# Kernel tuning notes

Measured on AMD Instinct MI355X. Metric: run time of the kernel, lower is better.

## Reference

```python
import jax, jax.numpy as jnp
import numpy as np

N = 200000   # nodes
E = 6400000  # edges (avg degree 32)
T = 6        # member feature dim
M = 10       # fingerprint dim
L = 4        # R + 1 layers
GIN = 14     # group_level_input
GLO = 10     # group_level_output


def setup_inputs() -> dict:
    key = jax.random.key(0)
    ks = jax.random.split(key, 10)
    return {
        "x_member": jax.random.normal(ks[0], (N, T), dtype=jnp.float32),
        "x_group": jax.random.normal(ks[1], (1, GIN), dtype=jnp.float32),
        "src": jax.random.randint(ks[2], (E,), 0, N, dtype=jnp.int32),
        "dst": jax.random.randint(ks[3], (E,), 0, N, dtype=jnp.int32),
        "H": jax.random.normal(ks[4], (L, T, M), dtype=jnp.float32),
        "W": jax.random.normal(ks[5], (L,), dtype=jnp.float32),
        "gW": jax.random.normal(ks[6], (GLO, GIN), dtype=jnp.float32) * 0.1,
        "gb": jax.random.normal(ks[7], (GLO,), dtype=jnp.float32),
        "mW": jax.random.normal(ks[8], (3, M + GLO), dtype=jnp.float32) * 0.1,
        "mb": jax.random.normal(ks[9], (3,), dtype=jnp.float32),
    }


def reference(x_member, x_group, src, dst, H, W, gW, gb, mW, mb):
    n = x_member.shape[0]
    # message passing: neighbor feature sum per destination node  [N, T]
    neigh = jax.ops.segment_sum(x_member[src], dst, num_segments=n)
    v1 = x_member + neigh  # r[a] + sum of neighbor r's; r is layer-invariant
    # all R+1 layers at once: [L, N, M]
    v2 = jax.nn.sigmoid(jnp.einsum("nt,ltm->lnm", v1, H))
    fl = jax.nn.softmax(v2 * W[:, None, None], axis=-1)
    # f starts at zeros and accumulates softmax over every node and layer -> [1, M]
    f = jnp.sum(fl, axis=(0, 1))[None, :]
    # group-level perceptron
    g = jax.nn.sigmoid(x_group @ gW.T + gb)  # [1, GLO]
    merged = jnp.concatenate([f, g], axis=1)  # [1, M+GLO]
    return jax.nn.softmax(merged @ mW.T + mb, axis=-1)  # [1, 3]
```

## Files before the change

kernel.cpp:

```cpp
#include <hip/hip_runtime.h>
#include <hip/hip_fp16.h>
#include <math.h>

#define TDIM 6
#define MDIM 10
#define LDIM 4
#define GIND 14
#define GLOD 10

#define BINSHIFT 8
#define BINSZ 256
#define MAXBINS 1024

#define SC2_BLOCKS 512
#define SC2_THREADS 512
#define SC2_KQ 7
#define OVF_ENT 16384
#define META2 2048

#define SC_BLOCK 512
#define SC_EPT 32
#define SC_EPB (SC_BLOCK * SC_EPT)
#define AC_BLOCK 512
#define AC_CAP 8704
#define AC_EPT 17

typedef unsigned uvec4_t __attribute__((ext_vector_type(4)));

__device__ __forceinline__ void add_row4(uint4 r, float& s0, float& s1, float& s2,
                                         float& s3, float& s4, float& s5) {
    float2 a0 = __half22float2(*(__half2*)&r.x);
    float2 a1 = __half22float2(*(__half2*)&r.y);
    float2 a2 = __half22float2(*(__half2*)&r.z);
    s0 += a0.x; s1 += a0.y; s2 += a1.x; s3 += a1.y; s4 += a2.x; s5 += a2.y;
}

__global__ void zero32_k(unsigned* __restrict__ p, int n) {
    int i = blockIdx.x * blockDim.x + threadIdx.x;
    if (i < n) p[i] = 0u;
}


__global__ __launch_bounds__(SC2_THREADS) void scat2_k(
        const float* __restrict__ xm, int N, uint4* __restrict__ xh,
        const int* __restrict__ src, const int* __restrict__ dst, int E, int NQ, int QPB,
        unsigned* __restrict__ gcount, unsigned* __restrict__ ebuf, int C, int nbins,
        uint2* __restrict__ ovf, unsigned* __restrict__ ocur) {
    __shared__ unsigned lcount[MAXBINS];
    __shared__ unsigned lbase[MAXBINS];
    int tid = threadIdx.x;
    for (int i = tid; i < MAXBINS; i += SC2_THREADS) lcount[i] = 0u;

    int gid = blockIdx.x * SC2_THREADS + tid;
    int gstride = gridDim.x * SC2_THREADS;
    for (int n = gid; n < N; n += gstride) {
        const float2* r = (const float2*)(xm + (size_t)n * TDIM);
        float2 a = r[0], b = r[1], c = r[2];
        __half2 h0 = __floats2half2_rn(a.x, a.y);
        __half2 h1 = __floats2half2_rn(b.x, b.y);
        __half2 h2 = __floats2half2_rn(c.x, c.y);
        uint4 o;
        o.x = *(unsigned*)&h0; o.y = *(unsigned*)&h1; o.z = *(unsigned*)&h2; o.w = 0u;
        xh[n] = o;
    }
    if (blockIdx.x == 0) {
        for (int e = NQ * 4 + tid; e < E; e += SC2_THREADS) {
            unsigned oc = atomicAdd(ocur, 1u);
            if (oc < OVF_ENT) ovf[oc] = make_uint2((unsigned)src[e], (unsigned)dst[e]);
        }
    }
    __syncthreads();

    int qb = blockIdx.x * QPB;
    int qend = qb + QPB; if (qend > NQ) qend = NQ;
    const int4* s4p = (const int4*)src;
    const int4* d4p = (const int4*)dst;

    unsigned pk[SC2_KQ * 4];
    unsigned wr[SC2_KQ * 4];

#pragma unroll
    for (int i = 0; i < SC2_KQ; i++) {
        int q = qb + tid + i * SC2_THREADS;
        if (q < qend) {
            int4 sv = s4p[q];
            int4 dv = d4p[q];
            {
                unsigned du = (unsigned)dv.x, b = du >> BINSHIFT;
                pk[i*4+0] = ((du & (BINSZ-1)) << 18) | (unsigned)sv.x;
                wr[i*4+0] = (b << 18) | atomicAdd(&lcount[b], 1u);
            }
            {
                unsigned du = (unsigned)dv.y, b = du >> BINSHIFT;
                pk[i*4+1] = ((du & (BINSZ-1)) << 18) | (unsigned)sv.y;
                wr[i*4+1] = (b << 18) | atomicAdd(&lcount[b], 1u);
            }
            {
                unsigned du = (unsigned)dv.z, b = du >> BINSHIFT;
                pk[i*4+2] = ((du & (BINSZ-1)) << 18) | (unsigned)sv.z;
                wr[i*4+2] = (b << 18) | atomicAdd(&lcount[b], 1u);
            }
            {
                unsigned du = (unsigned)dv.w, b = du >> BINSHIFT;
                pk[i*4+3] = ((du & (BINSZ-1)) << 18) | (unsigned)sv.w;
                wr[i*4+3] = (b << 18) | atomicAdd(&lcount[b], 1u);
            }
        } else {
            pk[i*4+0] = 0xFFFFFFFFu; pk[i*4+1] = 0xFFFFFFFFu;
            pk[i*4+2] = 0xFFFFFFFFu; pk[i*4+3] = 0xFFFFFFFFu;
        }
    }
    __syncthreads();

    for (int i = tid; i < nbins; i += SC2_THREADS) {
        unsigned c = lcount[i];
        if (c) lbase[i] = atomicAdd(&gcount[i], c);
    }
    __syncthreads();

#pragma unroll
    for (int k = 0; k < SC2_KQ * 4; k++) {
        unsigned p = pk[k];
        if (p != 0xFFFFFFFFu) {
            unsigned b = wr[k] >> 18;
            unsigned pos = lbase[b] + (wr[k] & 0x3FFFFu);
            if (pos < (unsigned)C) {
                ebuf[b * (unsigned)C + pos] = p;
            } else {
                unsigned oc = atomicAdd(ocur, 1u);
                if (oc < OVF_ENT) {
                    unsigned s = p & 0x3FFFFu;
                    unsigned d = (b << BINSHIFT) | (p >> 18);
                    ovf[oc] = make_uint2(s, d);
                }
            }
        }
    }
}

__global__ __launch_bounds__(AC_BLOCK) void accum2_k(
        const float* __restrict__ xm, const uint4* __restrict__ xh,
        const unsigned* __restrict__ ebuf, const unsigned* __restrict__ gcount, int C,
        const unsigned* __restrict__ ocur, const uint2* __restrict__ ovf,
        const float* __restrict__ H, const float* __restrict__ W,
        float* __restrict__ facc, int N) {
    __shared__ unsigned srt[AC_CAP];
    __shared__ unsigned cnt[BINSZ];
    __shared__ unsigned tmp[BINSZ];
    __shared__ unsigned cstart[BINSZ];
    __shared__ unsigned ovl[256];
    __shared__ unsigned ovn;
    __shared__ float sH[LDIM * TDIM * MDIM];
    __shared__ float sW[LDIM];
    __shared__ float sred[AC_BLOCK / 64][MDIM];
    __shared__ float part[2][BINSZ][TDIM];
    int tid = threadIdx.x;
    int bin = blockIdx.x;
    for (int i = tid; i < LDIM * TDIM * MDIM; i += AC_BLOCK) sH[i] = H[i];
    if (tid < LDIM) sW[tid] = W[tid];
    if (tid < BINSZ) cnt[tid] = 0u;
    if (tid == 0) ovn = 0u;
    __syncthreads();

    unsigned gc = gcount[bin];
    unsigned m = gc < (unsigned)C ? gc : (unsigned)C;
    unsigned e0 = (unsigned)bin * (unsigned)C;
    int nbase = bin << BINSHIFT;

    unsigned ed_[AC_EPT];
    unsigned rk_[AC_EPT];
#pragma unroll
    for (int k = 0; k < AC_EPT; k++) {
        unsigned i = (unsigned)tid + (unsigned)k * AC_BLOCK;
        if (i < m) {
            unsigned v = __builtin_nontemporal_load(ebuf + e0 + i);
            ed_[k] = v;
            rk_[k] = atomicAdd(&cnt[v >> 18], 1u);
        }
    }
    {
        unsigned novf = *ocur;
        if (novf > OVF_ENT) novf = OVF_ENT;
        for (unsigned i = tid; i < novf; i += AC_BLOCK) {
            uint2 e = ovf[i];
            if ((e.y >> BINSHIFT) == (unsigned)bin) {
                unsigned u = atomicAdd(&ovn, 1u);
                if (u < 256u) ovl[u] = ((e.y & (BINSZ-1)) << 18) | e.x;
            }
        }
    }
    __syncthreads();

    if (tid < BINSZ) tmp[tid] = cnt[tid];
    __syncthreads();
    for (int off = 1; off < BINSZ; off <<= 1) {
        unsigned v = 0;
        if (tid < BINSZ) { v = tmp[tid]; if (tid >= off) v += tmp[tid - off]; }
        __syncthreads();
        if (tid < BINSZ) tmp[tid] = v;
        __syncthreads();
    }
    if (tid < BINSZ) cstart[tid] = tmp[tid] - cnt[tid];
    __syncthreads();

#pragma unroll
    for (int k = 0; k < AC_EPT; k++) {
        unsigned i = (unsigned)tid + (unsigned)k * AC_BLOCK;
        if (i < m) {
            unsigned v = ed_[k];
            srt[cstart[v >> 18] + rk_[k]] = v & 0x3FFFFu;
        }
    }
    __syncthreads();

    int node = tid & (BINSZ - 1);
    int role = tid >> 8;
    int n = nbase + node;
    float s0 = 0.f, s1 = 0.f, s2 = 0.f, s3 = 0.f, s4 = 0.f, s5 = 0.f;
    if (n < N) {
        unsigned c = cnt[node];
        unsigned b0 = cstart[node];
        unsigned h = c >> 1;
        unsigned j  = role ? h : 0u;
        unsigned je = role ? c : h;
        for (; j + 4 <= je; j += 4) {
            unsigned ia = srt[b0 + j],     ib = srt[b0 + j + 1];
            unsigned ic = srt[b0 + j + 2], id = srt[b0 + j + 3];
            uint4 ra = xh[ia];
            uint4 rb = xh[ib];
            uint4 rc = xh[ic];
            uint4 rd = xh[id];
            add_row4(ra, s0, s1, s2, s3, s4, s5);
            add_row4(rb, s0, s1, s2, s3, s4, s5);
            add_row4(rc, s0, s1, s2, s3, s4, s5);
            add_row4(rd, s0, s1, s2, s3, s4, s5);
        }
        for (; j < je; ++j) {
            uint4 ra = xh[srt[b0 + j]];
            add_row4(ra, s0, s1, s2, s3, s4, s5);
        }
        if (role == 0) {
            unsigned no = ovn < 256u ? ovn : 256u;
            for (unsigned q = 0; q < no; q++) {
                unsigned o = ovl[q];
                if ((int)(o >> 18) == node) {
                    uint4 rr = xh[o & 0x3FFFFu];
                    add_row4(rr, s0, s1, s2, s3, s4, s5);
                }
            }
        }
    }
    part[role][node][0] = s0; part[role][node][1] = s1; part[role][node][2] = s2;
    part[role][node][3] = s3; part[role][node][4] = s4; part[role][node][5] = s5;
    __syncthreads();

    float fs[MDIM];
#pragma unroll
    for (int mm = 0; mm < MDIM; mm++) fs[mm] = 0.f;

    if (n < N) {
        float v[TDIM];
        const float2* xr = (const float2*)(xm + (size_t)n * TDIM);
        float2 x0 = xr[0], x1 = xr[1], x2 = xr[2];
        v[0] = x0.x + part[0][node][0] + part[1][node][0];
        v[1] = x0.y + part[0][node][1] + part[1][node][1];
        v[2] = x1.x + part[0][node][2] + part[1][node][2];
        v[3] = x1.y + part[0][node][3] + part[1][node][3];
        v[4] = x2.x + part[0][node][4] + part[1][node][4];
        v[5] = x2.y + part[0][node][5] + part[1][node][5];

        int lb = role << 1;
#pragma unroll
        for (int li = 0; li < 2; li++) {
            int l = lb + li;
            float z[MDIM];
#pragma unroll
            for (int mm = 0; mm < MDIM; mm++) {
                float a2 = 0.f;
#pragma unroll
                for (int t = 0; t < TDIM; t++) a2 += v[t] * sH[(l * TDIM + t) * MDIM + mm];
                z[mm] = a2;
            }
            float wl = sW[l];
            float mx = -1e30f;
#pragma unroll
            for (int mm = 0; mm < MDIM; mm++) {
                float sg = wl / (1.f + __expf(-z[mm]));
                z[mm] = sg;
                mx = fmaxf(mx, sg);
            }
            float se = 0.f;
#pragma unroll
            for (int mm = 0; mm < MDIM; mm++) {
                float e = __expf(z[mm] - mx);
                z[mm] = e;
                se += e;
            }
            float inv = 1.f / se;
#pragma unroll
            for (int mm = 0; mm < MDIM; mm++) fs[mm] += z[mm] * inv;
        }
    }

#pragma unroll
    for (int mm = 0; mm < MDIM; mm++) {
        float v = fs[mm];
#pragma unroll
        for (int off = 32; off > 0; off >>= 1) v += __shfl_down(v, off, 64);
        fs[mm] = v;
    }
    int wave = tid >> 6, lane = tid & 63;
    if (lane == 0) {
#pragma unroll
        for (int mm = 0; mm < MDIM; mm++) sred[wave][mm] = fs[mm];
    }
    __syncthreads();
    if (tid < MDIM) {
        float s = 0.f;
#pragma unroll
        for (int w = 0; w < AC_BLOCK / 64; w++) s += sred[w][tid];
        atomicAdd(facc + tid, s);
    }
}


__global__ __launch_bounds__(256) void prep_k(const float* __restrict__ xm, int N,
                                              uint4* __restrict__ xh,
                                              const int* __restrict__ dst, int E,
                                              unsigned* __restrict__ hist, int nbins) {
    __shared__ unsigned lh[MAXBINS];
    for (int i = threadIdx.x; i < MAXBINS; i += blockDim.x) lh[i] = 0u;
    __syncthreads();
    int gid = blockIdx.x * blockDim.x + threadIdx.x;
    int gstride = gridDim.x * blockDim.x;
    for (int n = gid; n < N; n += gstride) {
        const float2* r = (const float2*)(xm + (size_t)n * TDIM);
        float2 a = r[0], b = r[1], c = r[2];
        __half2 h0 = __floats2half2_rn(a.x, a.y);
        __half2 h1 = __floats2half2_rn(b.x, b.y);
        __half2 h2 = __floats2half2_rn(c.x, c.y);
        uint4 o;
        o.x = *(unsigned*)&h0; o.y = *(unsigned*)&h1; o.z = *(unsigned*)&h2; o.w = 0u;
        xh[n] = o;
    }
    int e4 = E >> 2;
    const int4* d4p = (const int4*)dst;
    for (int i = gid; i < e4; i += gstride) {
        int4 d = d4p[i];
        atomicAdd(&lh[((unsigned)d.x) >> BINSHIFT], 1u);
        atomicAdd(&lh[((unsigned)d.y) >> BINSHIFT], 1u);
        atomicAdd(&lh[((unsigned)d.z) >> BINSHIFT], 1u);
        atomicAdd(&lh[((unsigned)d.w) >> BINSHIFT], 1u);
    }
    for (int e = (e4 << 2) + gid; e < E; e += gstride)
        atomicAdd(&lh[((unsigned)dst[e]) >> BINSHIFT], 1u);
    __syncthreads();
    for (int i = threadIdx.x; i < nbins; i += blockDim.x)
        if (lh[i]) atomicAdd(&hist[i], lh[i]);
}

__global__ __launch_bounds__(MAXBINS) void scan_k(const unsigned* __restrict__ hist,
                                                  unsigned* __restrict__ offsets,
                                                  unsigned* __restrict__ gfill, int nbins) {
    __shared__ unsigned buf[2][MAXBINS];
    int t = threadIdx.x;
    buf[0][t] = (t < nbins) ? hist[t] : 0u;
    __syncthreads();
    int cur = 0;
    for (int off = 1; off < MAXBINS; off <<= 1) {
        unsigned v = buf[cur][t];
        if (t >= off) v += buf[cur][t - off];
        buf[cur ^ 1][t] = v;
        __syncthreads();
        cur ^= 1;
    }
    if (t < nbins) {
        unsigned ex = t ? buf[cur][t - 1] : 0u;
        offsets[t] = ex;
        gfill[t] = ex;
    }
    if (t == 0) offsets[nbins] = buf[cur][nbins - 1];
}

__global__ __launch_bounds__(SC_BLOCK) void scatter_k(const int* __restrict__ src,
                                                      const int* __restrict__ dst, int E,
                                                      unsigned* __restrict__ gfill,
                                                      unsigned* __restrict__ ebuf, int nbins) {
    __shared__ unsigned lcount[MAXBINS];
    __shared__ unsigned lbase[MAXBINS];
    for (int i = threadIdx.x; i < MAXBINS; i += SC_BLOCK) lcount[i] = 0u;
    __syncthreads();
    int base = blockIdx.x * SC_EPB + threadIdx.x * SC_EPT;
    int s[SC_EPT], d[SC_EPT];
    unsigned rk[SC_EPT];
#pragma unroll
    for (int q = 0; q < SC_EPT / 4; q++) {
        int e = base + q * 4;
        if (e + 3 < E) {
            int4 s4 = *(const int4*)(src + e);
            int4 d4 = *(const int4*)(dst + e);
            s[q*4+0] = s4.x; s[q*4+1] = s4.y; s[q*4+2] = s4.z; s[q*4+3] = s4.w;
            d[q*4+0] = d4.x; d[q*4+1] = d4.y; d[q*4+2] = d4.z; d[q*4+3] = d4.w;
        } else {
#pragma unroll
            for (int k = 0; k < 4; k++) {
                int ee = e + k;
                s[q*4+k] = (ee < E) ? src[ee] : -1;
                d[q*4+k] = (ee < E) ? dst[ee] : 0;
            }
        }
    }
#pragma unroll
    for (int k = 0; k < SC_EPT; k++)
        if (s[k] >= 0) rk[k] = atomicAdd(&lcount[((unsigned)d[k]) >> BINSHIFT], 1u);
    __syncthreads();
    for (int i = threadIdx.x; i < nbins; i += SC_BLOCK) {
        unsigned c = lcount[i];
        if (c) lbase[i] = atomicAdd(&gfill[i], c);
    }
    __syncthreads();
#pragma unroll
    for (int k = 0; k < SC_EPT; k++) {
        if (s[k] >= 0) {
            unsigned du = (unsigned)d[k];
            unsigned b = du >> BINSHIFT;
            unsigned pack = ((du & (BINSZ - 1)) << 18) | (unsigned)s[k];
            ebuf[lbase[b] + rk[k]] = pack;
        }
    }
}

__global__ __launch_bounds__(AC_BLOCK) void accum_node_k(
        const float* __restrict__ xm, const uint4* __restrict__ xh,
        const unsigned* __restrict__ ebuf, const unsigned* __restrict__ offsets,
        const float* __restrict__ H, const float* __restrict__ W,
        float* __restrict__ facc, int N) {
    __shared__ unsigned srt[AC_CAP];
    __shared__ unsigned cnt[BINSZ];
    __shared__ unsigned tmp[BINSZ];
    __shared__ unsigned cstart[BINSZ];
    __shared__ float sH[LDIM * TDIM * MDIM];
    __shared__ float sW[LDIM];
    __shared__ float sred[AC_BLOCK / 64][MDIM];
    int tid = threadIdx.x;
    int bin = blockIdx.x;
    for (int i = tid; i < LDIM * TDIM * MDIM; i += AC_BLOCK) sH[i] = H[i];
    if (tid < LDIM) sW[tid] = W[tid];
    if (tid < BINSZ) cnt[tid] = 0u;
    __syncthreads();

    unsigned e0 = offsets[bin], e1 = offsets[bin + 1];
    unsigned total = e1 - e0;
    unsigned m = total < AC_CAP ? total : AC_CAP;
    int nbase = bin << BINSHIFT;

    unsigned ed_[AC_EPT];
    unsigned rk_[AC_EPT];
#pragma unroll
    for (int k = 0; k < AC_EPT; k++) {
        unsigned idx = e0 + (unsigned)tid + (unsigned)k * AC_BLOCK;
        if (idx < e0 + m) {
            unsigned v = ebuf[idx];
            ed_[k] = v;
            rk_[k] = atomicAdd(&cnt[v >> 18], 1u);
        }
    }
    __syncthreads();

    if (tid < BINSZ) tmp[tid] = cnt[tid];
    __syncthreads();
    for (int off = 1; off < BINSZ; off <<= 1) {
        unsigned v = 0;
        if (tid < BINSZ) { v = tmp[tid]; if (tid >= off) v += tmp[tid - off]; }
        __syncthreads();
        if (tid < BINSZ) tmp[tid] = v;
        __syncthreads();
    }
    if (tid < BINSZ) cstart[tid] = tmp[tid] - cnt[tid];
    __syncthreads();

#pragma unroll
    for (int k = 0; k < AC_EPT; k++) {
        unsigned idx = e0 + (unsigned)tid + (unsigned)k * AC_BLOCK;
        if (idx < e0 + m) {
            unsigned v = ed_[k];
            srt[cstart[v >> 18] + rk_[k]] = v & 0x3FFFFu;
        }
    }
    __syncthreads();

    float fs[MDIM];
#pragma unroll
    for (int mm = 0; mm < MDIM; mm++) fs[mm] = 0.f;

    int n = nbase + tid;
    if (tid < BINSZ && n < N) {
        float s0 = 0.f, s1 = 0.f, s2 = 0.f, s3 = 0.f, s4 = 0.f, s5 = 0.f;
        unsigned c = cnt[tid];
        unsigned b0 = cstart[tid];
        unsigned j = 0;
        for (; j + 2 <= c; j += 2) {
            unsigned sa = srt[b0 + j], sb = srt[b0 + j + 1];
            uint4 ra = xh[sa];
            uint4 rb = xh[sb];
            float2 a0 = __half22float2(*(__half2*)&ra.x);
            float2 a1 = __half22float2(*(__half2*)&ra.y);
            float2 a2 = __half22float2(*(__half2*)&ra.z);
            float2 c0 = __half22float2(*(__half2*)&rb.x);
            float2 c1 = __half22float2(*(__half2*)&rb.y);
            float2 c2 = __half22float2(*(__half2*)&rb.z);
            s0 += a0.x + c0.x; s1 += a0.y + c0.y;
            s2 += a1.x + c1.x; s3 += a1.y + c1.y;
            s4 += a2.x + c2.x; s5 += a2.y + c2.y;
        }
        if (j < c) {
            uint4 ra = xh[srt[b0 + j]];
            float2 a0 = __half22float2(*(__half2*)&ra.x);
            float2 a1 = __half22float2(*(__half2*)&ra.y);
            float2 a2 = __half22float2(*(__half2*)&ra.z);
            s0 += a0.x; s1 += a0.y; s2 += a1.x; s3 += a1.y; s4 += a2.x; s5 += a2.y;
        }
        for (unsigned idx = e0 + m; idx < e1; idx++) {
            unsigned v = ebuf[idx];
            if ((int)(v >> 18) == tid) {
                uint4 ra = xh[v & 0x3FFFFu];
                float2 a0 = __half22float2(*(__half2*)&ra.x);
                float2 a1 = __half22float2(*(__half2*)&ra.y);
                float2 a2 = __half22float2(*(__half2*)&ra.z);
                s0 += a0.x; s1 += a0.y; s2 += a1.x; s3 += a1.y; s4 += a2.x; s5 += a2.y;
            }
        }

        float v[TDIM];
        const float2* xr = (const float2*)(xm + (size_t)n * TDIM);
        float2 x0 = xr[0], x1 = xr[1], x2 = xr[2];
        v[0] = x0.x + s0; v[1] = x0.y + s1;
        v[2] = x1.x + s2; v[3] = x1.y + s3;
        v[4] = x2.x + s4; v[5] = x2.y + s5;

#pragma unroll
        for (int l = 0; l < LDIM; l++) {
            float z[MDIM];
#pragma unroll
            for (int mm = 0; mm < MDIM; mm++) {
                float a2 = 0.f;
#pragma unroll
                for (int t = 0; t < TDIM; t++) a2 += v[t] * sH[(l * TDIM + t) * MDIM + mm];
                z[mm] = a2;
            }
            float wl = sW[l];
            float mx = -1e30f;
#pragma unroll
            for (int mm = 0; mm < MDIM; mm++) {
                float sg = wl / (1.f + __expf(-z[mm]));
                z[mm] = sg;
                mx = fmaxf(mx, sg);
            }
            float se = 0.f;
#pragma unroll
            for (int mm = 0; mm < MDIM; mm++) {
                float e = __expf(z[mm] - mx);
                z[mm] = e;
                se += e;
            }
            float inv = 1.f / se;
#pragma unroll
            for (int mm = 0; mm < MDIM; mm++) fs[mm] += z[mm] * inv;
        }
    }

#pragma unroll
    for (int mm = 0; mm < MDIM; mm++) {
        float v = fs[mm];
#pragma unroll
        for (int off = 32; off > 0; off >>= 1) v += __shfl_down(v, off, 64);
        fs[mm] = v;
    }
    int wave = tid >> 6, lane = tid & 63;
    if (lane == 0) {
#pragma unroll
        for (int mm = 0; mm < MDIM; mm++) sred[wave][mm] = fs[mm];
    }
    __syncthreads();
    if (tid < MDIM) {
        float s = 0.f;
#pragma unroll
        for (int w = 0; w < AC_BLOCK / 64; w++) s += sred[w][tid];
        atomicAdd(facc + tid, s);
    }
}

__global__ void finalize_k(const float* __restrict__ facc,
                           const float* __restrict__ xg,
                           const float* __restrict__ gW,
                           const float* __restrict__ gb,
                           const float* __restrict__ mW,
                           const float* __restrict__ mb,
                           float* __restrict__ out) {
    if (threadIdx.x == 0 && blockIdx.x == 0) {
        float merged[MDIM + GLOD];
#pragma unroll
        for (int m = 0; m < MDIM; m++) merged[m] = facc[m];
        for (int j = 0; j < GLOD; j++) {
            float a = gb[j];
            for (int i = 0; i < GIND; i++) a += xg[i] * gW[j * GIND + i];
            merged[MDIM + j] = 1.f / (1.f + __expf(-a));
        }
        float lg[3];
        float mx = -1e30f;
        for (int k = 0; k < 3; k++) {
            float a = mb[k];
            for (int j = 0; j < MDIM + GLOD; j++) a += merged[j] * mW[k * (MDIM + GLOD) + j];
            lg[k] = a;
            mx = fmaxf(mx, a);
        }
        float se = 0.f;
        for (int k = 0; k < 3; k++) { lg[k] = __expf(lg[k] - mx); se += lg[k]; }
        float inv = 1.f / se;
        for (int k = 0; k < 3; k++) out[k] = lg[k] * inv;
    }
}

__global__ void fb_zero_k(float* __restrict__ ws, int n) {
    int i = blockIdx.x * blockDim.x + threadIdx.x;
    if (i < n) ws[i] = 0.f;
}

__global__ void fb_edge_scatter_k(const float* __restrict__ xm,
                                  const int* __restrict__ src,
                                  const int* __restrict__ dst,
                                  float* __restrict__ neigh, int E) {
    int e = blockIdx.x * blockDim.x + threadIdx.x;
    if (e >= E) return;
    int s = src[e], d = dst[e];
    const float2* r = (const float2*)(xm + (size_t)s * TDIM);
    float2 a = r[0], b = r[1], c = r[2];
    float* o = neigh + (size_t)d * TDIM;
    atomicAdd(o + 0, a.x); atomicAdd(o + 1, a.y);
    atomicAdd(o + 2, b.x); atomicAdd(o + 3, b.y);
    atomicAdd(o + 4, c.x); atomicAdd(o + 5, c.y);
}

__global__ __launch_bounds__(256) void fb_node_k(
        const float* __restrict__ xm, const float* __restrict__ neigh,
        const float* __restrict__ H, const float* __restrict__ W,
        float* __restrict__ facc, int N) {
    __shared__ float sH[LDIM * TDIM * MDIM];
    __shared__ float sW[LDIM];
    __shared__ float sred[4][MDIM];
    int tid = threadIdx.x;
    for (int i = tid; i < LDIM * TDIM * MDIM; i += blockDim.x) sH[i] = H[i];
    if (tid < LDIM) sW[tid] = W[tid];
    __syncthreads();
    float fs[MDIM];
#pragma unroll
    for (int m = 0; m < MDIM; m++) fs[m] = 0.f;
    for (int n = blockIdx.x * blockDim.x + tid; n < N; n += gridDim.x * blockDim.x) {
        float v[TDIM];
        const float2* xr = (const float2*)(xm + (size_t)n * TDIM);
        const float2* nr = (const float2*)(neigh + (size_t)n * TDIM);
#pragma unroll
        for (int t2 = 0; t2 < 3; t2++) {
            float2 a = xr[t2], b = nr[t2];
            v[2 * t2 + 0] = a.x + b.x;
            v[2 * t2 + 1] = a.y + b.y;
        }
#pragma unroll
        for (int l = 0; l < LDIM; l++) {
            float z[MDIM];
#pragma unroll
            for (int m = 0; m < MDIM; m++) {
                float a2 = 0.f;
#pragma unroll
                for (int t = 0; t < TDIM; t++) a2 += v[t] * sH[(l * TDIM + t) * MDIM + m];
                z[m] = a2;
            }
            float wl = sW[l], mx = -1e30f;
#pragma unroll
            for (int m = 0; m < MDIM; m++) { float sg = wl / (1.f + __expf(-z[m])); z[m] = sg; mx = fmaxf(mx, sg); }
            float se = 0.f;
#pragma unroll
            for (int m = 0; m < MDIM; m++) { float e = __expf(z[m] - mx); z[m] = e; se += e; }
            float inv = 1.f / se;
#pragma unroll
            for (int m = 0; m < MDIM; m++) fs[m] += z[m] * inv;
        }
    }
#pragma unroll
    for (int m = 0; m < MDIM; m++) {
        float v = fs[m];
#pragma unroll
        for (int off = 32; off > 0; off >>= 1) v += __shfl_down(v, off, 64);
        fs[m] = v;
    }
    int wave = tid >> 6, lane = tid & 63;
    if (lane == 0) {
#pragma unroll
        for (int m = 0; m < MDIM; m++) sred[wave][m] = fs[m];
    }
    __syncthreads();
    if (tid < MDIM) {
        float s = sred[0][tid] + sred[1][tid] + sred[2][tid] + sred[3][tid];
        atomicAdd(facc + tid, s);
    }
}

extern "C" void kernel_launch(void* const* d_in, const int* in_sizes, int n_in,
                              void* d_out, int out_size, void* d_ws, size_t ws_size,
                              hipStream_t stream) {
    const float* xm  = (const float*)d_in[0];
    const float* xg  = (const float*)d_in[1];
    const int*   src = (const int*)d_in[2];
    const int*   dst = (const int*)d_in[3];
    const float* H   = (const float*)d_in[4];
    const float* W   = (const float*)d_in[5];
    const float* gW  = (const float*)d_in[6];
    const float* gb  = (const float*)d_in[7];
    const float* mW  = (const float*)d_in[8];
    const float* mb  = (const float*)d_in[9];
    float* out = (float*)d_out;

    int N = in_sizes[0] / TDIM;
    int E = in_sizes[2];
    int nbins = (N + BINSZ - 1) >> BINSHIFT;
    size_t ws_words = ws_size / 4;
    size_t xh_words = (size_t)N * 4;

    long fixed = (long)(xh_words + META2 + (size_t)OVF_ENT * 2);
    long avail = (long)ws_words - fixed;
    long C = avail > 0 ? (avail / nbins) & ~3L : 0;
    if (C > AC_CAP) C = AC_CAP;
    double mu = (double)E / nbins;
    long Cmin = (long)(mu + 4.0 * sqrt(mu) + 32.0);
    int NQ = E >> 2;
    int QPB = (NQ + SC2_BLOCKS - 1) / SC2_BLOCKS;
    bool ok1 = (C >= Cmin) && nbins <= MAXBINS && N <= (1 << 18) &&
               QPB <= SC2_KQ * SC2_THREADS;

    size_t meta_words2 = MAXBINS + (MAXBINS + 1) + MAXBINS + 16;
    size_t need2 = (xh_words + (size_t)E + meta_words2) * 4;
    bool ok2 = ws_size >= need2 && nbins <= MAXBINS && N <= (1 << 18);

    if (ok1) {
        uint4*    xh     = (uint4*)d_ws;
        unsigned* ebuf   = (unsigned*)d_ws + xh_words;
        unsigned* gcount = ebuf + (size_t)nbins * C;
        unsigned* ocur   = gcount + MAXBINS;
        float*    facc   = (float*)(ocur + 16);
        uint2*    ovf    = (uint2*)(gcount + META2);

        zero32_k<<<(META2 + 255) / 256, 256, 0, stream>>>(gcount, META2);
        scat2_k<<<SC2_BLOCKS, SC2_THREADS, 0, stream>>>(xm, N, xh, src, dst, E, NQ, QPB,
                                                        gcount, ebuf, (int)C, nbins, ovf, ocur);
        accum2_k<<<nbins, AC_BLOCK, 0, stream>>>(xm, xh, ebuf, gcount, (int)C, ocur, ovf,
                                                 H, W, facc, N);
        finalize_k<<<1, 64, 0, stream>>>(facc, xg, gW, gb, mW, mb, out);
    } else if (ok2) {
        uint4*    xh      = (uint4*)d_ws;
        unsigned* ebuf    = (unsigned*)d_ws + xh_words;
        unsigned* hist    = ebuf + (size_t)E;
        unsigned* offsets = hist + MAXBINS;
        unsigned* gfill   = offsets + MAXBINS + 1;
        float*    facc    = (float*)(gfill + MAXBINS);

        zero32_k<<<(int)((meta_words2 + 255) / 256), 256, 0, stream>>>(hist, (int)meta_words2);
        prep_k<<<1024, 256, 0, stream>>>(xm, N, xh, dst, E, hist, nbins);
        scan_k<<<1, MAXBINS, 0, stream>>>(hist, offsets, gfill, nbins);
        scatter_k<<<(E + SC_EPB - 1) / SC_EPB, SC_BLOCK, 0, stream>>>(src, dst, E, gfill, ebuf, nbins);
        accum_node_k<<<nbins, AC_BLOCK, 0, stream>>>(xm, xh, ebuf, offsets, H, W, facc, N);
        finalize_k<<<1, 64, 0, stream>>>(facc, xg, gW, gb, mW, mb, out);
    } else {
        float* neigh = (float*)d_ws;
        float* facc  = neigh + (size_t)N * TDIM;
        int zn = N * TDIM + 16;
        fb_zero_k<<<(zn + 255) / 256, 256, 0, stream>>>(neigh, zn);
        fb_edge_scatter_k<<<(E + 255) / 256, 256, 0, stream>>>(xm, src, dst, neigh, E);
        fb_node_k<<<256, 256, 0, stream>>>(xm, neigh, H, W, facc, N);
        finalize_k<<<1, 64, 0, stream>>>(facc, xg, gW, gb, mW, mb, out);
    }
}
```

Before: 138.0 us.

## Replace per-bin counting sort with LDS float atomic accumulation

The accumulate kernel no longer counting-sorts each bin's edges by destination node (histogram, scan, scatter) before a per-node gather loop. Each thread now reads edges four at a time with vector loads, gathers the fp16 source rows, and adds them straight into a padded shared-memory float accumulator with atomics. Overflow edges are also added directly. This drops several barriers, the scan, and the large sort buffer, which may raise occupancy. The cost is six LDS float atomics per edge, with contention on popular nodes, and a summation order that is no longer deterministic.

```diff
diff --git a/kernel.cpp b/kernel.cpp
--- a/kernel.cpp
+++ b/kernel.cpp
@@ -25,15 +25,9 @@
 #define AC_CAP 8704
 #define AC_EPT 17
 
+#define ACC_PAD 7
+
 typedef unsigned uvec4_t __attribute__((ext_vector_type(4)));
-
-__device__ __forceinline__ void add_row4(uint4 r, float& s0, float& s1, float& s2,
-                                         float& s3, float& s4, float& s5) {
-    float2 a0 = __half22float2(*(__half2*)&r.x);
-    float2 a1 = __half22float2(*(__half2*)&r.y);
-    float2 a2 = __half22float2(*(__half2*)&r.z);
-    s0 += a0.x; s1 += a0.y; s2 += a1.x; s3 += a1.y; s4 += a2.x; s5 += a2.y;
-}
 
 __global__ void zero32_k(unsigned* __restrict__ p, int n) {
     int i = blockIdx.x * blockDim.x + threadIdx.x;
@@ -144,39 +138,56 @@
         const unsigned* __restrict__ ocur, const uint2* __restrict__ ovf,
         const float* __restrict__ H, const float* __restrict__ W,
         float* __restrict__ facc, int N) {
-    __shared__ unsigned srt[AC_CAP];
-    __shared__ unsigned cnt[BINSZ];
-    __shared__ unsigned tmp[BINSZ];
-    __shared__ unsigned cstart[BINSZ];
-    __shared__ unsigned ovl[256];
-    __shared__ unsigned ovn;
+    __shared__ float acc[BINSZ][ACC_PAD];
     __shared__ float sH[LDIM * TDIM * MDIM];
     __shared__ float sW[LDIM];
     __shared__ float sred[AC_BLOCK / 64][MDIM];
-    __shared__ float part[2][BINSZ][TDIM];
     int tid = threadIdx.x;
     int bin = blockIdx.x;
     for (int i = tid; i < LDIM * TDIM * MDIM; i += AC_BLOCK) sH[i] = H[i];
     if (tid < LDIM) sW[tid] = W[tid];
-    if (tid < BINSZ) cnt[tid] = 0u;
-    if (tid == 0) ovn = 0u;
+    for (int i = tid; i < BINSZ * ACC_PAD; i += AC_BLOCK) ((float*)acc)[i] = 0.f;
     __syncthreads();
 
     unsigned gc = gcount[bin];
     unsigned m = gc < (unsigned)C ? gc : (unsigned)C;
-    unsigned e0 = (unsigned)bin * (unsigned)C;
-    int nbase = bin << BINSHIFT;
-
-    unsigned ed_[AC_EPT];
-    unsigned rk_[AC_EPT];
-#pragma unroll
-    for (int k = 0; k < AC_EPT; k++) {
-        unsigned i = (unsigned)tid + (unsigned)k * AC_BLOCK;
-        if (i < m) {
-            unsigned v = __builtin_nontemporal_load(ebuf + e0 + i);
-            ed_[k] = v;
-            rk_[k] = atomicAdd(&cnt[v >> 18], 1u);
-        }
+    const unsigned* eb = ebuf + (size_t)bin * (unsigned)C;
+
+    unsigned m4 = m >> 2;
+    const uvec4_t* eb4 = (const uvec4_t*)eb;
+    for (unsigned q = tid; q < m4; q += AC_BLOCK) {
+        uvec4_t e4 = __builtin_nontemporal_load(eb4 + q);
+        unsigned va[4] = {e4[0], e4[1], e4[2], e4[3]};
+        uint4 r[4];
+#pragma unroll
+        for (int k = 0; k < 4; k++) r[k] = xh[va[k] & 0x3FFFFu];
+#pragma unroll
+        for (int k = 0; k < 4; k++) {
+            unsigned node = va[k] >> 18;
+            float2 a0 = __half22float2(*(__half2*)&r[k].x);
+            float2 a1 = __half22float2(*(__half2*)&r[k].y);
+            float2 a2 = __half22float2(*(__half2*)&r[k].z);
+            atomicAdd(&acc[node][0], a0.x);
+            atomicAdd(&acc[node][1], a0.y);
+            atomicAdd(&acc[node][2], a1.x);
+            atomicAdd(&acc[node][3], a1.y);
+            atomicAdd(&acc[node][4], a2.x);
+            atomicAdd(&acc[node][5], a2.y);
+        }
+    }
+    for (unsigned i = (m4 << 2) + tid; i < m; i += AC_BLOCK) {
+        unsigned v = eb[i];
+        unsigned node = v >> 18;
+        uint4 r = xh[v & 0x3FFFFu];
+        float2 a0 = __half22float2(*(__half2*)&r.x);
+        float2 a1 = __half22float2(*(__half2*)&r.y);
+        float2 a2 = __half22float2(*(__half2*)&r.z);
+        atomicAdd(&acc[node][0], a0.x);
+        atomicAdd(&acc[node][1], a0.y);
+        atomicAdd(&acc[node][2], a1.x);
+        atomicAdd(&acc[node][3], a1.y);
+        atomicAdd(&acc[node][4], a2.x);
+        atomicAdd(&acc[node][5], a2.y);
     }
     {
         unsigned novf = *ocur;
@@ -184,75 +195,25 @@
         for (unsigned i = tid; i < novf; i += AC_BLOCK) {
             uint2 e = ovf[i];
             if ((e.y >> BINSHIFT) == (unsigned)bin) {
-                unsigned u = atomicAdd(&ovn, 1u);
-                if (u < 256u) ovl[u] = ((e.y & (BINSZ-1)) << 18) | e.x;
-            }
-        }
-    }
-    __syncthreads();
-
-    if (tid < BINSZ) tmp[tid] = cnt[tid];
-    __syncthreads();
-    for (int off = 1; off < BINSZ; off <<= 1) {
-        unsigned v = 0;
-        if (tid < BINSZ) { v = tmp[tid]; if (tid >= off) v += tmp[tid - off]; }
-        __syncthreads();
-        if (tid < BINSZ) tmp[tid] = v;
-        __syncthreads();
-    }
-    if (tid < BINSZ) cstart[tid] = tmp[tid] - cnt[tid];
-    __syncthreads();
-
-#pragma unroll
-    for (int k = 0; k < AC_EPT; k++) {
-        unsigned i = (unsigned)tid + (unsigned)k * AC_BLOCK;
-        if (i < m) {
-            unsigned v = ed_[k];
-            srt[cstart[v >> 18] + rk_[k]] = v & 0x3FFFFu;
+                unsigned node = e.y & (BINSZ - 1);
+                uint4 r = xh[e.x];
+                float2 a0 = __half22float2(*(__half2*)&r.x);
+                float2 a1 = __half22float2(*(__half2*)&r.y);
+                float2 a2 = __half22float2(*(__half2*)&r.z);
+                atomicAdd(&acc[node][0], a0.x);
+                atomicAdd(&acc[node][1], a0.y);
+                atomicAdd(&acc[node][2], a1.x);
+                atomicAdd(&acc[node][3], a1.y);
+                atomicAdd(&acc[node][4], a2.x);
+                atomicAdd(&acc[node][5], a2.y);
+            }
         }
     }
     __syncthreads();
 
     int node = tid & (BINSZ - 1);
     int role = tid >> 8;
-    int n = nbase + node;
-    float s0 = 0.f, s1 = 0.f, s2 = 0.f, s3 = 0.f, s4 = 0.f, s5 = 0.f;
-    if (n < N) {
-        unsigned c = cnt[node];
-        unsigned b0 = cstart[node];
-        unsigned h = c >> 1;
-        unsigned j  = role ? h : 0u;
-        unsigned je = role ? c : h;
-        for (; j + 4 <= je; j += 4) {
-            unsigned ia = srt[b0 + j],     ib = srt[b0 + j + 1];
-            unsigned ic = srt[b0 + j + 2], id = srt[b0 + j + 3];
-            uint4 ra = xh[ia];
-            uint4 rb = xh[ib];
-            uint4 rc = xh[ic];
-            uint4 rd = xh[id];
-            add_row4(ra, s0, s1, s2, s3, s4, s5);
-            add_row4(rb, s0, s1, s2, s3, s4, s5);
-            add_row4(rc, s0, s1, s2, s3, s4, s5);
-            add_row4(rd, s0, s1, s2, s3, s4, s5);
-        }
-        for (; j < je; ++j) {
-            uint4 ra = xh[srt[b0 + j]];
-            add_row4(ra, s0, s1, s2, s3, s4, s5);
-        }
-        if (role == 0) {
-            unsigned no = ovn < 256u ? ovn : 256u;
-            for (unsigned q = 0; q < no; q++) {
-                unsigned o = ovl[q];
-                if ((int)(o >> 18) == node) {
-                    uint4 rr = xh[o & 0x3FFFFu];
-                    add_row4(rr, s0, s1, s2, s3, s4, s5);
-                }
-            }
-        }
-    }
-    part[role][node][0] = s0; part[role][node][1] = s1; part[role][node][2] = s2;
-    part[role][node][3] = s3; part[role][node][4] = s4; part[role][node][5] = s5;
-    __syncthreads();
+    int n = (bin << BINSHIFT) + node;
 
     float fs[MDIM];
 #pragma unroll
@@ -262,12 +223,9 @@
         float v[TDIM];
         const float2* xr = (const float2*)(xm + (size_t)n * TDIM);
         float2 x0 = xr[0], x1 = xr[1], x2 = xr[2];
-        v[0] = x0.x + part[0][node][0] + part[1][node][0];
-        v[1] = x0.y + part[0][node][1] + part[1][node][1];
-        v[2] = x1.x + part[0][node][2] + part[1][node][2];
-        v[3] = x1.y + part[0][node][3] + part[1][node][3];
-        v[4] = x2.x + part[0][node][4] + part[1][node][4];
-        v[5] = x2.y + part[0][node][5] + part[1][node][5];
+        v[0] = x0.x + acc[node][0]; v[1] = x0.y + acc[node][1];
+        v[2] = x1.x + acc[node][2]; v[3] = x1.y + acc[node][3];
+        v[4] = x2.x + acc[node][4]; v[5] = x2.y + acc[node][5];
 
         int lb = role << 1;
 #pragma unroll
```

Result: slower. 341.9 us (+147.8%).
